# Kernel tuning notes

Measured on AMD Instinct MI355X. Metric: run time of the kernel, lower is better.

The kernel has to match this reference:

```python
import jax, jax.numpy as jnp
import numpy as np

A, H, HI = 4, 3, 2  # nagents, n_pol_heads, n_intr_rew_heads (sep_extr_head=True)
# leave-one-out index table: row i lists all agents k != i, in ascending order (torch loop order)
LOO = np.array([[k for k in range(A) if k != i] for i in range(A)])  # [A, A-1]


def setup_inputs() -> dict:
    key = jax.random.key(0)
    ks = jax.random.split(key, 12)
    B, S, C, D = 32768, 256, 16, 128  # batch, vect_state_size, action_size, hidden_dim
    IN = C * (A - 1) + D  # 176 critic input dim
    r = lambda k, shp, s=0.05: jax.random.normal(k, shp, dtype=jnp.float32) * s
    return {
        "state_vect": jax.random.normal(ks[0], (B, S), dtype=jnp.float32),
        "acs": jax.random.normal(ks[1], (A, H, B, C), dtype=jnp.float32),
        "enc_W": r(ks[2], (S, D)),
        "enc_b": r(ks[3], (D,)),
        "extr_W1": r(ks[4], (H, A, IN, D)),
        "extr_b1": r(ks[5], (H, A, D)),
        "extr_W2": r(ks[6], (H, A, D, C)),
        "extr_b2": r(ks[7], (H, A, C)),
        "intr_W1": r(ks[8], (HI, A, IN, D)),
        "intr_b1": r(ks[9], (HI, A, D)),
        "intr_W2": r(ks[10], (HI, A, D, C)),
        "intr_b2": r(ks[11], (HI, A, C)),
    }


def reference(state_vect, acs, enc_W, enc_b, extr_W1, extr_b1, extr_W2, extr_b2,
              intr_W1, intr_b1, intr_W2, intr_b2):
    B, C = acs.shape[2], acs.shape[3]
    D = enc_W.shape[1]
    # shared state encoder: Linear -> ReLU
    enc = jax.nn.relu(state_vect @ enc_W + enc_b)  # [B, D]
    # leave-one-out action concat per (agent, head): cat(acs[k!=i, j]) ++ enc
    rel = acs[LOO]                                 # [A, A-1, H, B, C]
    rel = rel.transpose(0, 2, 3, 1, 4).reshape(A, H, B, (A - 1) * C)
    x = jnp.concatenate([rel, jnp.broadcast_to(enc, (A, H, B, D))], axis=-1)  # [A,H,B,IN]
    # greedy action index of agent i's own head-j policy output
    int_acs = jnp.argmax(acs, axis=-1)             # [A, H, B]

    def critic(xin, W1, b1, W2, b2):
        # xin: [A, Hc, B, IN]; W1: [Hc, A, IN, D]; W2: [Hc, A, D, C]
        h = jax.nn.relu(jnp.einsum('ahbi,haid->ahbd', xin, W1)
                        + b1.transpose(1, 0, 2)[:, :, None, :])
        return (jnp.einsum('ahbd,hadc->ahbc', h, W2)
                + b2.transpose(1, 0, 2)[:, :, None, :])  # [A, Hc, B, C]

    extr_all_q = critic(x, extr_W1, extr_b1, extr_W2, extr_b2)          # [A,H,B,C]
    extr_q = jnp.take_along_axis(extr_all_q, int_acs[..., None], axis=-1)  # [A,H,B,1]
    # intr critics exist only for heads j>=1 (sep_extr_head=True -> offset -1)
    intr_all_q = critic(x[:, 1:], intr_W1, intr_b1, intr_W2, intr_b2)   # [A,HI,B,C]
    intr_q = jnp.take_along_axis(intr_all_q, int_acs[:, 1:, :, None], axis=-1)  # [A,HI,B,1]
    return extr_q, intr_q
```

## Files before the change

kernel.cpp:

```cpp
#include <hip/hip_runtime.h>

#define NA 4
#define NH 3
#define NHI 2
#define Bsz 32768
#define Ssz 256
#define Csz 16
#define Dsz 128
#define INsz 176
#define NP 20
#define KP 192
#define GT 4

typedef __bf16 v8bf __attribute__((ext_vector_type(8)));
typedef float v4f __attribute__((ext_vector_type(4)));

#define OFF_ENC    0
#define OFF_ACSBF  8388608
#define OFF_W1F    20971520
#define OFF_ENCWF  21954560
#define OFF_W2T    22020096
#define OFF_AMX    22102016
#define OFF_ZERO   22495232

#define N_ACSROW (NA*NH*Bsz)
#define N_W1F   (NP*192*32)
#define N_ENCWF (256*32)
#define N_W2T   (NP*Csz*Dsz)
#define N_ZERO  16
#define N_PREP  (N_ACSROW+N_W1F+N_ENCWF+N_W2T+N_ZERO)

__global__ __launch_bounds__(256) void prep_kernel(
    const float* __restrict__ acs, const float* __restrict__ encW,
    const float* __restrict__ eW1, const float* __restrict__ iW1,
    const float* __restrict__ eW2, const float* __restrict__ iW2,
    const float* __restrict__ eb1, const float* __restrict__ ib1,
    char* __restrict__ ws)
{
    long tid = (long)blockIdx.x * 256 + threadIdx.x;

    if (tid < N_ACSROW) {
        const float4* src = (const float4*)(acs + (size_t)tid * 16);
        float4 f0 = src[0], f1 = src[1], f2 = src[2], f3 = src[3];
        float v[16] = {f0.x,f0.y,f0.z,f0.w, f1.x,f1.y,f1.z,f1.w,
                       f2.x,f2.y,f2.z,f2.w, f3.x,f3.y,f3.z,f3.w};
        v8bf o0, o1;
        #pragma unroll
        for (int i = 0; i < 8; ++i) { o0[i] = (__bf16)v[i]; o1[i] = (__bf16)v[8 + i]; }
        const int plane = (int)(tid >> 15);
        const int b     = (int)(tid & 32767);
        const int rt    = b >> 4, mm = b & 15;
        char* dstb = ws + OFF_ACSBF + (size_t)plane * 1048576 + (size_t)rt * 512 + mm * 16;
        *(v8bf*)dstb         = o0;
        *(v8bf*)(dstb + 256) = o1;
        float best = v[0]; int bi = 0;
        #pragma unroll
        for (int c = 1; c < 16; ++c) if (v[c] > best) { best = v[c]; bi = c; }
        const int grp = b >> 6, mt = (b >> 4) & 3, m = b & 15;
        ((unsigned char*)(ws + OFF_AMX))[(size_t)plane * 32768 + grp * 64 + m * 4 + mt]
            = (unsigned char)bi;
        return;
    }
    tid -= N_ACSROW;
    if (tid < N_W1F) {
        const int n4 = (int)(tid & 31) * 4;
        const int k  = (int)((tid >> 5) % 192);
        const int p  = (int)(tid / 6144);
        const float* W1; const float* B1;
        if (p < 12) { int ai = p / 3, hj = p % 3; int wi = hj * NA + ai;
                      W1 = eW1 + (size_t)wi * INsz * Dsz; B1 = eb1 + (size_t)wi * Dsz; }
        else { int qq = p - 12; int ai = qq >> 1, jj = qq & 1; int wi = jj * NA + ai;
               W1 = iW1 + (size_t)wi * INsz * Dsz; B1 = ib1 + (size_t)wi * Dsz; }
        float4 f;
        if (k < 128)        f = *(const float4*)(W1 + (size_t)(48 + k) * Dsz + n4);
        else if (k < INsz)  f = *(const float4*)(W1 + (size_t)(k - 128) * Dsz + n4);
        else if (k == INsz) f = *(const float4*)(B1 + n4);
        else                f = (float4){0.f, 0.f, 0.f, 0.f};
        const int kc = k >> 5, q = (k >> 3) & 3, j = k & 7;
        __bf16* dst = (__bf16*)(ws + OFF_W1F);
        const float fv[4] = {f.x, f.y, f.z, f.w};
        #pragma unroll
        for (int i = 0; i < 4; ++i) {
            const int n = n4 + i, nt = n >> 4, m = n & 15;
            dst[((size_t)(p * 6 + kc) * 8 + nt) * 512 + (q * 16 + m) * 8 + j] = (__bf16)fv[i];
        }
        return;
    }
    tid -= N_W1F;
    if (tid < N_ENCWF) {
        const int n4 = (int)(tid & 31) * 4;
        const int k  = (int)(tid >> 5);
        float4 f = *(const float4*)(encW + (size_t)k * Dsz + n4);
        const int kc = k >> 5, q = (k >> 3) & 3, j = k & 7;
        __bf16* dst = (__bf16*)(ws + OFF_ENCWF);
        const float fv[4] = {f.x, f.y, f.z, f.w};
        #pragma unroll
        for (int i = 0; i < 4; ++i) {
            const int n = n4 + i, nt = n >> 4, m = n & 15;
            dst[((size_t)kc * 8 + nt) * 512 + (q * 16 + m) * 8 + j] = (__bf16)fv[i];
        }
        return;
    }
    tid -= N_ENCWF;
    if (tid < N_W2T) {
        int d = (int)(tid & 127);
        int rest = (int)(tid >> 7);
        int c = rest & 15, p = rest >> 4;
        const float* W2;
        if (p < 12) { int ai = p / 3, hj = p % 3; W2 = eW2 + (size_t)(hj * NA + ai) * Dsz * Csz; }
        else { int qq = p - 12; int ai = qq >> 1, jj = qq & 1; W2 = iW2 + (size_t)(jj * NA + ai) * Dsz * Csz; }
        const int dlow = d & 15, dt = d >> 4;
        ((__bf16*)(ws + OFF_W2T))[(size_t)p * 2048 + c * 128 + ((dlow ^ c) * 8) + dt]
            = (__bf16)W2[(size_t)d * Csz + c];
        return;
    }
    tid -= N_W2T;
    if (tid < N_ZERO) {
        ((unsigned int*)(ws + OFF_ZERO))[tid] = (tid == 0) ? 0x00003F80u : 0u;
    }
}

__global__ __launch_bounds__(256) void enc_kernel(const float* __restrict__ sv,
                                                  const float* __restrict__ encb,
                                                  char* __restrict__ ws)
{
    __shared__ __bf16 svs[64][264];
    __shared__ __bf16 tb[4][16 * 136];

    const int t = threadIdx.x;
    const int wv = t >> 6, lane = t & 63, m = lane & 15, q = lane >> 4;
    const __bf16* encwf = (const __bf16*)(ws + OFF_ENCWF);
    char* enct = ws + OFF_ENC;

    {
        const float* src = sv + ((size_t)blockIdx.x * 64 + wv * 16) * Ssz;
        #pragma unroll
        for (int i = 0; i < 16; ++i) {
            float4 f = *(const float4*)(src + i * Ssz + lane * 4);
            __bf16* d = &svs[wv * 16 + i][lane * 4];
            d[0] = (__bf16)f.x; d[1] = (__bf16)f.y; d[2] = (__bf16)f.z; d[3] = (__bf16)f.w;
        }
    }

    v4f acc[8];
    #pragma unroll
    for (int nt = 0; nt < 8; ++nt) acc[nt] = (v4f){0.f, 0.f, 0.f, 0.f};

    #pragma unroll
    for (int kc = 0; kc < 8; ++kc) {
        v8bf af = *(const v8bf*)&svs[wv * 16 + m][kc * 32 + q * 8];
        #pragma unroll
        for (int nt = 0; nt < 8; ++nt) {
            v8bf bf = *(const v8bf*)(encwf + ((size_t)kc * 8 + nt) * 512 + lane * 8);
            acc[nt] = __builtin_amdgcn_mfma_f32_16x16x32_bf16(af, bf, acc[nt], 0, 0, 0);
        }
    }
    #pragma unroll
    for (int nt = 0; nt < 8; ++nt) {
        const float bias = encb[nt * 16 + m];
        #pragma unroll
        for (int rg = 0; rg < 4; ++rg) {
            float v = acc[nt][rg] + bias;
            v = v > 0.f ? v : 0.f;
            tb[wv][(q * 4 + rg) * 136 + nt * 16 + m] = (__bf16)v;
        }
    }
    const int rt = blockIdx.x * 4 + wv;
    #pragma unroll
    for (int kc = 0; kc < 4; ++kc) {
        v8bf v = *(const v8bf*)&tb[wv][m * 136 + kc * 32 + q * 8];
        *(v8bf*)(enct + ((size_t)(rt * 4 + kc) * 64 + lane) * 16) = v;
    }
}

#define LD_E(D, KC, GG) \
  { _Pragma("unroll") \
    for (int mt_ = 0; mt_ < 4; ++mt_) \
      D[mt_] = *(const v8bf*)(encL + (GG) * 65536 + mt_ * 4096 + (KC) * 1024); }

#define LD_4(D, GG) \
  { _Pragma("unroll") \
    for (int mt_ = 0; mt_ < 4; ++mt_) \
      D[mt_] = *(const v8bf*)(a4L + (GG) * 8192 + mt_ * 512); }

#define LD_5(D, GG) \
  { _Pragma("unroll") \
    for (int mt_ = 0; mt_ < 4; ++mt_) \
      D[mt_] = *(const v8bf*)(a5L + (GG) * g5 + mt_ * s5); }

#define MFMA_KC(AF, KC) \
  { __builtin_amdgcn_s_setprio(1); \
    _Pragma("unroll") \
    for (int nt_ = 0; nt_ < 8; ++nt_) { \
      v8bf bf_ = *(const v8bf*)&w1s[(size_t)(((KC) * 8 + nt_) * 512) + lane * 8]; \
      acc[0][nt_] = __builtin_amdgcn_mfma_f32_16x16x32_bf16(bf_, AF[0], acc[0][nt_], 0, 0, 0); \
      acc[1][nt_] = __builtin_amdgcn_mfma_f32_16x16x32_bf16(bf_, AF[1], acc[1][nt_], 0, 0, 0); \
      acc[2][nt_] = __builtin_amdgcn_mfma_f32_16x16x32_bf16(bf_, AF[2], acc[2][nt_], 0, 0, 0); \
      acc[3][nt_] = __builtin_amdgcn_mfma_f32_16x16x32_bf16(bf_, AF[3], acc[3][nt_], 0, 0, 0); \
    } \
    __builtin_amdgcn_s_setprio(0); }

#define EPILOG(GG) \
  { _Pragma("unroll") \
    for (int mt = 0; mt < 4; ++mt) { \
        const int c = (int)((cw >> (8 * mt)) & 255u); \
        const __bf16* wcb = &w2s[c * 128]; \
        float s0 = 0.f, s1 = 0.f; \
        _Pragma("unroll") \
        for (int rg = 0; rg < 4; rg += 2) { \
            const v8bf wa = *(const v8bf*)&wcb[((q * 4 + rg) ^ c) * 8]; \
            const v8bf wb = *(const v8bf*)&wcb[((q * 4 + rg + 1) ^ c) * 8]; \
            _Pragma("unroll") \
            for (int nt = 0; nt < 8; ++nt) { \
                s0 += fmaxf(acc[mt][nt][rg],     0.f) * (float)wa[nt]; \
                s1 += fmaxf(acc[mt][nt][rg + 1], 0.f) * (float)wb[nt]; \
            } \
        } \
        float tsum = s0 + s1; \
        tsum += __shfl_xor(tsum, 16, 64); \
        tsum += __shfl_xor(tsum, 32, 64); \
        if (q == 0) \
            outp[(size_t)rb * 1024 + (GG) * 256 + wv * 64 + mt * 16 + m] = tsum + b2s[c]; \
        if ((GG) + 1 < GT) { \
            _Pragma("unroll") \
            for (int nt = 0; nt < 8; ++nt) acc[mt][nt] = (v4f){0.f, 0.f, 0.f, 0.f}; \
        } \
    } }

#define GBODY(GG, A_, B_, C_, D_, LAST) \
  { const unsigned int cw = *(const unsigned int*)(amxL + (GG) * 256); \
    LD_E(D_, 3, GG)                      MFMA_KC(A_, 0) \
    LD_4(A_, GG)                         MFMA_KC(B_, 1) \
    LD_5(B_, GG)                         MFMA_KC(C_, 2) \
    if (!(LAST)) { LD_E(C_, 0, (GG)+1) } MFMA_KC(D_, 3) \
    if (!(LAST)) { LD_E(D_, 1, (GG)+1) } MFMA_KC(A_, 4) \
    if (!(LAST)) { LD_E(A_, 2, (GG)+1) } MFMA_KC(B_, 5) \
    EPILOG(GG) }

__global__ __launch_bounds__(256, 2) void critic_kernel(
    const float* __restrict__ eb2, const float* __restrict__ ib2,
    const char* __restrict__ ws, float* __restrict__ out)
{
    __shared__ __bf16 w1s[6 * 8 * 512];
    __shared__ __bf16 w2s[16 * 128];
    __shared__ float  b2s[16];

    const int t = threadIdx.x;
    const int p  = blockIdx.y;
    const int rb = blockIdx.x;
    const int wv = t >> 6, lane = t & 63, m = lane & 15, q = lane >> 4;

    int ai, hj;
    const float* b2;
    float* outp;
    if (p < 12) {
        ai = p / 3; hj = p % 3;
        b2 = eb2 + (size_t)(hj * NA + ai) * Csz;
        outp = out + (size_t)(ai * NH + hj) * Bsz;
    } else {
        const int qq = p - 12; ai = qq >> 1; const int jj = qq & 1; hj = jj + 1;
        b2 = ib2 + (size_t)(jj * NA + ai) * Csz;
        outp = out + (size_t)NA * NH * Bsz + (size_t)(ai * NHI + jj) * Bsz;
    }

    const __bf16* w1f = (const __bf16*)(ws + OFF_W1F) + (size_t)p * 6 * 8 * 512;
    const __bf16* w2t = (const __bf16*)(ws + OFF_W2T) + (size_t)p * 2048;
    const char* amxL = ws + OFF_AMX + (size_t)(ai * NH + hj) * 32768
        + ((size_t)rb * 16 + wv) * 64 + m * 4;

    {
        const v8bf* src = (const v8bf*)w1f;
        #pragma unroll
        for (int i = 0; i < 12; ++i)
            ((v8bf*)w1s)[i * 256 + t] = src[i * 256 + t];
        ((v8bf*)w2s)[t] = ((const v8bf*)w2t)[t];
        if (t < 16) b2s[t] = b2[t];
    }

    const int loo0 = 0 + (0 >= ai), loo1 = 1 + (1 >= ai), loo2 = 2 + (2 >= ai);
    const int pA = loo0 * NH + hj, pB = loo1 * NH + hj, pC = loo2 * NH + hj;
    const int rtb = rb * 64 + wv * 4;
    const char* encL = ws + OFF_ENC + (size_t)rtb * 4096 + lane * 16;
    const size_t rtoff = (size_t)rtb * 512 + (lane & 31) * 16;
    const char* a4L = ws + OFF_ACSBF + (size_t)((q < 2) ? pA : pB) * 1048576 + rtoff;
    const char* a5L; int s5, g5;
    if (q < 2) { a5L = ws + OFF_ACSBF + (size_t)pC * 1048576 + rtoff; s5 = 512; g5 = 8192; }
    else       { a5L = ws + OFF_ZERO + (q - 2) * 16;                  s5 = 0;   g5 = 0;    }

    v4f acc[4][8];
    #pragma unroll
    for (int i = 0; i < 4; ++i)
        #pragma unroll
        for (int j = 0; j < 8; ++j)
            acc[i][j] = (v4f){0.f, 0.f, 0.f, 0.f};

    v8bf af0[4], af1[4], af2[4], af3[4];
    LD_E(af0, 0, 0)
    LD_E(af1, 1, 0)
    LD_E(af2, 2, 0)

    __syncthreads();

    GBODY(0, af0, af1, af2, af3, 0)
    GBODY(1, af2, af3, af0, af1, 0)
    GBODY(2, af0, af1, af2, af3, 0)
    GBODY(3, af2, af3, af0, af1, 1)
}

extern "C" void kernel_launch(void* const* d_in, const int* in_sizes, int n_in,
                              void* d_out, int out_size, void* d_ws, size_t ws_size,
                              hipStream_t stream) {
    const float* sv   = (const float*)d_in[0];
    const float* acs  = (const float*)d_in[1];
    const float* encW = (const float*)d_in[2];
    const float* encb = (const float*)d_in[3];
    const float* eW1  = (const float*)d_in[4];
    const float* eb1  = (const float*)d_in[5];
    const float* eW2  = (const float*)d_in[6];
    const float* eb2  = (const float*)d_in[7];
    const float* iW1  = (const float*)d_in[8];
    const float* ib1  = (const float*)d_in[9];
    const float* iW2  = (const float*)d_in[10];
    const float* ib2  = (const float*)d_in[11];
    float* out = (float*)d_out;
    char* ws = (char*)d_ws;

    hipLaunchKernelGGL(prep_kernel, dim3((N_PREP + 255) / 256), dim3(256), 0, stream,
                       acs, encW, eW1, iW1, eW2, iW2, eb1, ib1, ws);
    hipLaunchKernelGGL(enc_kernel, dim3(Bsz / 64), dim3(256), 0, stream, sv, encb, ws);
    hipLaunchKernelGGL(critic_kernel, dim3(Bsz / 1024, NP), dim3(256), 0, stream,
                       eb2, ib2, ws, out);
}
```

Baseline: 160.6 us.

## Halve rows per critic block and stagger K-chunk order across blocks

Each critic block now handles 512 rows instead of 1024, which doubles the grid to 64x20 blocks for better occupancy and load balance. The main loop moves to a three-buffer rotation over K-chunks. Alternating blocks (by parity of rb+p) walk the K-chunks in a different starting order, so co-resident blocks hit the encoder and action data at different times, meant to spread memory traffic. In exchange, the per-block preload of W1/W2 into shared memory is amortised over half as many rows, and there is less prefetch depth.

```diff
diff --git a/kernel.cpp b/kernel.cpp
--- a/kernel.cpp
+++ b/kernel.cpp
@@ -10,7 +10,7 @@
 #define INsz 176
 #define NP 20
 #define KP 192
-#define GT 4
+#define GT 2
 
 typedef __bf16 v8bf __attribute__((ext_vector_type(8)));
 typedef float v4f __attribute__((ext_vector_type(4)));
@@ -220,22 +220,12 @@
         tsum += __shfl_xor(tsum, 16, 64); \
         tsum += __shfl_xor(tsum, 32, 64); \
         if (q == 0) \
-            outp[(size_t)rb * 1024 + (GG) * 256 + wv * 64 + mt * 16 + m] = tsum + b2s[c]; \
+            outp[(size_t)rb * 512 + (GG) * 256 + wv * 64 + mt * 16 + m] = tsum + b2s[c]; \
         if ((GG) + 1 < GT) { \
             _Pragma("unroll") \
             for (int nt = 0; nt < 8; ++nt) acc[mt][nt] = (v4f){0.f, 0.f, 0.f, 0.f}; \
         } \
     } }
-
-#define GBODY(GG, A_, B_, C_, D_, LAST) \
-  { const unsigned int cw = *(const unsigned int*)(amxL + (GG) * 256); \
-    LD_E(D_, 3, GG)                      MFMA_KC(A_, 0) \
-    LD_4(A_, GG)                         MFMA_KC(B_, 1) \
-    LD_5(B_, GG)                         MFMA_KC(C_, 2) \
-    if (!(LAST)) { LD_E(C_, 0, (GG)+1) } MFMA_KC(D_, 3) \
-    if (!(LAST)) { LD_E(D_, 1, (GG)+1) } MFMA_KC(A_, 4) \
-    if (!(LAST)) { LD_E(A_, 2, (GG)+1) } MFMA_KC(B_, 5) \
-    EPILOG(GG) }
 
 __global__ __launch_bounds__(256, 2) void critic_kernel(
     const float* __restrict__ eb2, const float* __restrict__ ib2,
@@ -266,7 +256,7 @@
     const __bf16* w1f = (const __bf16*)(ws + OFF_W1F) + (size_t)p * 6 * 8 * 512;
     const __bf16* w2t = (const __bf16*)(ws + OFF_W2T) + (size_t)p * 2048;
     const char* amxL = ws + OFF_AMX + (size_t)(ai * NH + hj) * 32768
-        + ((size_t)rb * 16 + wv) * 64 + m * 4;
+        + ((size_t)rb * 8 + wv) * 64 + m * 4;
 
     {
         const v8bf* src = (const v8bf*)w1f;
@@ -279,7 +269,7 @@
 
     const int loo0 = 0 + (0 >= ai), loo1 = 1 + (1 >= ai), loo2 = 2 + (2 >= ai);
     const int pA = loo0 * NH + hj, pB = loo1 * NH + hj, pC = loo2 * NH + hj;
-    const int rtb = rb * 64 + wv * 4;
+    const int rtb = rb * 32 + wv * 4;
     const char* encL = ws + OFF_ENC + (size_t)rtb * 4096 + lane * 16;
     const size_t rtoff = (size_t)rtb * 512 + (lane & 31) * 16;
     const char* a4L = ws + OFF_ACSBF + (size_t)((q < 2) ? pA : pB) * 1048576 + rtoff;
@@ -294,17 +284,43 @@
         for (int j = 0; j < 8; ++j)
             acc[i][j] = (v4f){0.f, 0.f, 0.f, 0.f};
 
-    v8bf af0[4], af1[4], af2[4], af3[4];
-    LD_E(af0, 0, 0)
-    LD_E(af1, 1, 0)
-    LD_E(af2, 2, 0)
-
-    __syncthreads();
-
-    GBODY(0, af0, af1, af2, af3, 0)
-    GBODY(1, af2, af3, af0, af1, 0)
-    GBODY(2, af0, af1, af2, af3, 0)
-    GBODY(3, af2, af3, af0, af1, 1)
+    v8bf af0[4], af1[4], af2[4];
+
+    if (((rb + p) & 1) == 0) {
+        LD_E(af0, 0, 0)
+        LD_E(af1, 1, 0)
+        __syncthreads();
+        #pragma unroll
+        for (int g = 0; g < GT; ++g) {
+            const unsigned int cw = *(const unsigned int*)(amxL + g * 256);
+            LD_E(af2, 2, g)  MFMA_KC(af0, 0)
+            LD_E(af0, 3, g)  MFMA_KC(af1, 1)
+            LD_4(af1, g)     MFMA_KC(af2, 2)
+            LD_5(af2, g)     MFMA_KC(af0, 3)
+            if (g + 1 < GT) { LD_E(af0, 0, g + 1) }
+            MFMA_KC(af1, 4)
+            if (g + 1 < GT) { LD_E(af1, 1, g + 1) }
+            MFMA_KC(af2, 5)
+            EPILOG(g)
+        }
+    } else {
+        LD_E(af0, 3, 0)
+        LD_4(af1, 0)
+        __syncthreads();
+        #pragma unroll
+        for (int g = 0; g < GT; ++g) {
+            const unsigned int cw = *(const unsigned int*)(amxL + g * 256);
+            LD_5(af2, g)     MFMA_KC(af0, 3)
+            LD_E(af0, 0, g)  MFMA_KC(af1, 4)
+            LD_E(af1, 1, g)  MFMA_KC(af2, 5)
+            LD_E(af2, 2, g)  MFMA_KC(af0, 0)
+            if (g + 1 < GT) { LD_E(af0, 3, g + 1) }
+            MFMA_KC(af1, 1)
+            if (g + 1 < GT) { LD_4(af1, g + 1) }
+            MFMA_KC(af2, 2)
+            EPILOG(g)
+        }
+    }
 }
 
 extern "C" void kernel_launch(void* const* d_in, const int* in_sizes, int n_in,
@@ -328,6 +344,6 @@
     hipLaunchKernelGGL(prep_kernel, dim3((N_PREP + 255) / 256), dim3(256), 0, stream,
                        acs, encW, eW1, iW1, eW2, iW2, eb1, ib1, ws);
     hipLaunchKernelGGL(enc_kernel, dim3(Bsz / 64), dim3(256), 0, stream, sv, encb, ws);
-    hipLaunchKernelGGL(critic_kernel, dim3(Bsz / 1024, NP), dim3(256), 0, stream,
+    hipLaunchKernelGGL(critic_kernel, dim3(Bsz / 512, NP), dim3(256), 0, stream,
                        eb2, ib2, ws, out);
 }
```

New measurement: 150.0 us. 6.6% less time.

## Split critic hidden dim into two halves to cut registers and raise occupancy

Applied to the files above, without the earlier changes.

The critic kernel now computes the 128-wide hidden layer in two 64-column halves. Each half's ReLU·W2 partial sum is accumulated before the next half runs, which halves the accumulator registers and removes two of the four A-fragment buffers. Launch bounds go from 2 to 3 blocks per CU, and each block covers 512 rows instead of 1024, doubling the grid. In exchange, the encoder and action fragments are reloaded for each half, and the deep prefetch pipeline across groups is reduced.

```diff
diff --git a/kernel.cpp b/kernel.cpp
--- a/kernel.cpp
+++ b/kernel.cpp
@@ -10,7 +10,7 @@
 #define INsz 176
 #define NP 20
 #define KP 192
-#define GT 4
+#define GT 2
 
 typedef __bf16 v8bf __attribute__((ext_vector_type(8)));
 typedef float v4f __attribute__((ext_vector_type(4)));
@@ -188,11 +188,11 @@
     for (int mt_ = 0; mt_ < 4; ++mt_) \
       D[mt_] = *(const v8bf*)(a5L + (GG) * g5 + mt_ * s5); }
 
-#define MFMA_KC(AF, KC) \
+#define MFMA_H(AF, KC, H) \
   { __builtin_amdgcn_s_setprio(1); \
     _Pragma("unroll") \
-    for (int nt_ = 0; nt_ < 8; ++nt_) { \
-      v8bf bf_ = *(const v8bf*)&w1s[(size_t)(((KC) * 8 + nt_) * 512) + lane * 8]; \
+    for (int nt_ = 0; nt_ < 4; ++nt_) { \
+      v8bf bf_ = *(const v8bf*)&w1s[(size_t)(((KC) * 8 + (H) * 4 + nt_) * 512) + lane * 8]; \
       acc[0][nt_] = __builtin_amdgcn_mfma_f32_16x16x32_bf16(bf_, AF[0], acc[0][nt_], 0, 0, 0); \
       acc[1][nt_] = __builtin_amdgcn_mfma_f32_16x16x32_bf16(bf_, AF[1], acc[1][nt_], 0, 0, 0); \
       acc[2][nt_] = __builtin_amdgcn_mfma_f32_16x16x32_bf16(bf_, AF[2], acc[2][nt_], 0, 0, 0); \
@@ -200,44 +200,52 @@
     } \
     __builtin_amdgcn_s_setprio(0); }
 
-#define EPILOG(GG) \
+#define PASS(GG, H, PRE_G, LAST) \
+  LD_E(af1, 1, GG)  MFMA_H(af0, 0, H) \
+  LD_E(af0, 2, GG)  MFMA_H(af1, 1, H) \
+  LD_E(af1, 3, GG)  MFMA_H(af0, 2, H) \
+  LD_4(af0, GG)     MFMA_H(af1, 3, H) \
+  LD_5(af1, GG)     MFMA_H(af0, 4, H) \
+  if (!(LAST)) { LD_E(af0, 0, PRE_G) } \
+  MFMA_H(af1, 5, H)
+
+#define ZACC \
+  { _Pragma("unroll") \
+    for (int i_ = 0; i_ < 4; ++i_) \
+        _Pragma("unroll") \
+        for (int j_ = 0; j_ < 4; ++j_) \
+            acc[i_][j_] = (v4f){0.f, 0.f, 0.f, 0.f}; }
+
+#define EPIPART(H) \
   { _Pragma("unroll") \
     for (int mt = 0; mt < 4; ++mt) { \
         const int c = (int)((cw >> (8 * mt)) & 255u); \
         const __bf16* wcb = &w2s[c * 128]; \
-        float s0 = 0.f, s1 = 0.f; \
         _Pragma("unroll") \
         for (int rg = 0; rg < 4; rg += 2) { \
             const v8bf wa = *(const v8bf*)&wcb[((q * 4 + rg) ^ c) * 8]; \
             const v8bf wb = *(const v8bf*)&wcb[((q * 4 + rg + 1) ^ c) * 8]; \
             _Pragma("unroll") \
-            for (int nt = 0; nt < 8; ++nt) { \
-                s0 += fmaxf(acc[mt][nt][rg],     0.f) * (float)wa[nt]; \
-                s1 += fmaxf(acc[mt][nt][rg + 1], 0.f) * (float)wb[nt]; \
+            for (int nt = 0; nt < 4; ++nt) { \
+                p0[mt] += fmaxf(acc[mt][nt][rg],     0.f) * (float)wa[(H) * 4 + nt]; \
+                p1[mt] += fmaxf(acc[mt][nt][rg + 1], 0.f) * (float)wb[(H) * 4 + nt]; \
             } \
         } \
-        float tsum = s0 + s1; \
+    } }
+
+#define EPIFINAL(GG) \
+  { _Pragma("unroll") \
+    for (int mt = 0; mt < 4; ++mt) { \
+        float tsum = p0[mt] + p1[mt]; \
         tsum += __shfl_xor(tsum, 16, 64); \
         tsum += __shfl_xor(tsum, 32, 64); \
-        if (q == 0) \
-            outp[(size_t)rb * 1024 + (GG) * 256 + wv * 64 + mt * 16 + m] = tsum + b2s[c]; \
-        if ((GG) + 1 < GT) { \
-            _Pragma("unroll") \
-            for (int nt = 0; nt < 8; ++nt) acc[mt][nt] = (v4f){0.f, 0.f, 0.f, 0.f}; \
+        if (q == 0) { \
+            const int c = (int)((cw >> (8 * mt)) & 255u); \
+            outp[(size_t)rb * 512 + (GG) * 256 + wv * 64 + mt * 16 + m] = tsum + b2s[c]; \
         } \
     } }
 
-#define GBODY(GG, A_, B_, C_, D_, LAST) \
-  { const unsigned int cw = *(const unsigned int*)(amxL + (GG) * 256); \
-    LD_E(D_, 3, GG)                      MFMA_KC(A_, 0) \
-    LD_4(A_, GG)                         MFMA_KC(B_, 1) \
-    LD_5(B_, GG)                         MFMA_KC(C_, 2) \
-    if (!(LAST)) { LD_E(C_, 0, (GG)+1) } MFMA_KC(D_, 3) \
-    if (!(LAST)) { LD_E(D_, 1, (GG)+1) } MFMA_KC(A_, 4) \
-    if (!(LAST)) { LD_E(A_, 2, (GG)+1) } MFMA_KC(B_, 5) \
-    EPILOG(GG) }
-
-__global__ __launch_bounds__(256, 2) void critic_kernel(
+__global__ __launch_bounds__(256, 3) void critic_kernel(
     const float* __restrict__ eb2, const float* __restrict__ ib2,
     const char* __restrict__ ws, float* __restrict__ out)
 {
@@ -266,7 +274,7 @@
     const __bf16* w1f = (const __bf16*)(ws + OFF_W1F) + (size_t)p * 6 * 8 * 512;
     const __bf16* w2t = (const __bf16*)(ws + OFF_W2T) + (size_t)p * 2048;
     const char* amxL = ws + OFF_AMX + (size_t)(ai * NH + hj) * 32768
-        + ((size_t)rb * 16 + wv) * 64 + m * 4;
+        + ((size_t)rb * 8 + wv) * 64 + m * 4;
 
     {
         const v8bf* src = (const v8bf*)w1f;
@@ -279,7 +287,7 @@
 
     const int loo0 = 0 + (0 >= ai), loo1 = 1 + (1 >= ai), loo2 = 2 + (2 >= ai);
     const int pA = loo0 * NH + hj, pB = loo1 * NH + hj, pC = loo2 * NH + hj;
-    const int rtb = rb * 64 + wv * 4;
+    const int rtb = rb * 32 + wv * 4;
     const char* encL = ws + OFF_ENC + (size_t)rtb * 4096 + lane * 16;
     const size_t rtoff = (size_t)rtb * 512 + (lane & 31) * 16;
     const char* a4L = ws + OFF_ACSBF + (size_t)((q < 2) ? pA : pB) * 1048576 + rtoff;
@@ -287,24 +295,34 @@
     if (q < 2) { a5L = ws + OFF_ACSBF + (size_t)pC * 1048576 + rtoff; s5 = 512; g5 = 8192; }
     else       { a5L = ws + OFF_ZERO + (q - 2) * 16;                  s5 = 0;   g5 = 0;    }
 
-    v4f acc[4][8];
-    #pragma unroll
-    for (int i = 0; i < 4; ++i)
-        #pragma unroll
-        for (int j = 0; j < 8; ++j)
-            acc[i][j] = (v4f){0.f, 0.f, 0.f, 0.f};
-
-    v8bf af0[4], af1[4], af2[4], af3[4];
+    v4f acc[4][4];
+    v8bf af0[4], af1[4];
+    float p0[4], p1[4];
+
     LD_E(af0, 0, 0)
-    LD_E(af1, 1, 0)
-    LD_E(af2, 2, 0)
-
     __syncthreads();
 
-    GBODY(0, af0, af1, af2, af3, 0)
-    GBODY(1, af2, af3, af0, af1, 0)
-    GBODY(2, af0, af1, af2, af3, 0)
-    GBODY(3, af2, af3, af0, af1, 1)
+    unsigned int cw = *(const unsigned int*)(amxL + 0);
+    #pragma unroll
+    for (int i = 0; i < 4; ++i) { p0[i] = 0.f; p1[i] = 0.f; }
+    ZACC
+    PASS(0, 0, 0, 0)
+    EPIPART(0)
+    ZACC
+    PASS(0, 1, 1, 0)
+    EPIPART(1)
+    EPIFINAL(0)
+
+    cw = *(const unsigned int*)(amxL + 256);
+    #pragma unroll
+    for (int i = 0; i < 4; ++i) { p0[i] = 0.f; p1[i] = 0.f; }
+    ZACC
+    PASS(1, 0, 1, 0)
+    EPIPART(0)
+    ZACC
+    PASS(1, 1, 0, 1)
+    EPIPART(1)
+    EPIFINAL(1)
 }
 
 extern "C" void kernel_launch(void* const* d_in, const int* in_sizes, int n_in,
@@ -328,6 +346,6 @@
     hipLaunchKernelGGL(prep_kernel, dim3((N_PREP + 255) / 256), dim3(256), 0, stream,
                        acs, encW, eW1, iW1, eW2, iW2, eb1, ib1, ws);
     hipLaunchKernelGGL(enc_kernel, dim3(Bsz / 64), dim3(256), 0, stream, sv, encb, ws);
-    hipLaunchKernelGGL(critic_kernel, dim3(Bsz / 1024, NP), dim3(256), 0, stream,
+    hipLaunchKernelGGL(critic_kernel, dim3(Bsz / 512, NP), dim3(256), 0, stream,
                        eb2, ib2, ws, out);
 }
```

Result: slower. 199.1 us (+24.0%).
